# Kernel tuning notes

Hardware: AMD Instinct MI355X
Metric: run time of the kernel (lower is better)

Reference implementation:

```python
import jax, jax.numpy as jnp
import numpy as np
from jax import lax

EMBED_DIM = 384
NUM_GROUPS = 128
GROUP_SIZE = 64
LN_EPS = 1e-5


def setup_inputs() -> dict:
    key = jax.random.key(0)
    k_pts, k1, k2, k3, k4 = jax.random.split(key, 5)
    B, N = 32, 16384
    points = jax.random.normal(k_pts, (B, N, 3), dtype=jnp.float32)
    # local_mlp: Linear(3,128) -> GELU -> Linear(128, embed_dim)
    w1 = jax.random.normal(k1, (3, 128), dtype=jnp.float32) * (1.0 / np.sqrt(3))
    b1 = jax.random.normal(k2, (128,), dtype=jnp.float32) * 0.01
    w2 = jax.random.normal(k3, (128, EMBED_DIM), dtype=jnp.float32) * (1.0 / np.sqrt(128))
    b2 = jax.random.normal(k4, (EMBED_DIM,), dtype=jnp.float32) * 0.01
    ln_scale = jnp.ones((EMBED_DIM,), dtype=jnp.float32)
    ln_bias = jnp.zeros((EMBED_DIM,), dtype=jnp.float32)
    return {"points": points, "w1": w1, "b1": b1, "w2": w2, "b2": b2,
            "ln_scale": ln_scale, "ln_bias": ln_bias}


def _farthest_point_sample(points, num_samples):
    # points: [B, N, 3]. Deterministic start at index 0 (torch uses randint).
    B, N, _ = points.shape

    def step(carry, _):
        distance, farthest = carry  # [B, N], [B]
        centroid = jnp.take_along_axis(points, farthest[:, None, None], axis=1)  # [B,1,3]
        d = jnp.sum((points - centroid) ** 2, axis=-1)  # [B, N]
        distance = jnp.minimum(distance, d)
        nxt = jnp.argmax(distance, axis=-1).astype(jnp.int32)
        return (distance, nxt), farthest

    init = (jnp.full((B, N), jnp.inf, dtype=points.dtype),
            jnp.zeros((B,), dtype=jnp.int32))
    _, idx = lax.scan(step, init, None, length=num_samples)  # [S, B]
    return idx.T  # [B, S]


def reference(points, w1, b1, w2, b2, ln_scale, ln_bias):
    B, N, _ = points.shape
    centroid_idx = _farthest_point_sample(points, NUM_GROUPS)  # [B, G]
    centroids = jnp.take_along_axis(
        points, centroid_idx[:, :, None].astype(jnp.int32), axis=1)  # [B, G, 3]

    # squared distances (same ordering as torch.cdist for topk); matmul form
    # avoids materializing a [B, G, N, 3] diff tensor.
    c2 = jnp.sum(centroids ** 2, axis=-1)  # [B, G]
    p2 = jnp.sum(points ** 2, axis=-1)     # [B, N]
    dist2 = c2[:, :, None] + p2[:, None, :] - 2.0 * jnp.einsum(
        'bgc,bnc->bgn', centroids, points)  # [B, G, N]

    # k smallest -> top_k of negated distances
    _, neighbor_idx = lax.top_k(-dist2, GROUP_SIZE)  # [B, G, K]

    batch_ix = jnp.arange(B)[:, None, None]
    grouped = points[batch_ix, neighbor_idx]  # [B, G, K, 3]
    local_coords = grouped - centroids[:, :, None, :]  # [B, G, K, 3]

    h = jax.nn.gelu(local_coords @ w1 + b1, approximate=False)  # [B,G,K,128]
    feats = h @ w2 + b2  # [B, G, K, D]
    tokens = jnp.mean(feats, axis=2)  # [B, G, D]

    mu = jnp.mean(tokens, axis=-1, keepdims=True)
    var = jnp.mean((tokens - mu) ** 2, axis=-1, keepdims=True)
    tokens_ln = (tokens - mu) * lax.rsqrt(var + LN_EPS) * ln_scale + ln_bias
    return centroids, tokens_ln
```

## Files before the change

kernel.cpp:

```cpp
#include <hip/hip_runtime.h>
#include <math.h>

#define BB 32
#define NN 16384
#define GG 128
#define KK 64
#define HH 128
#define DD 384
#define LN_EPS 1e-5f
#define NBUCK 2048
#define CANDCAP 1024

__device__ __forceinline__ float sq3(float x, float y, float z) {
    return __fadd_rn(__fadd_rn(__fmul_rn(x, x), __fmul_rn(y, y)), __fmul_rn(z, z));
}

__global__ void prep_kernel(const float* __restrict__ w2, float* __restrict__ w2t) {
    int i = blockIdx.x * 256 + threadIdx.x;
    if (i < HH * DD) {
        int f = i >> 7;
        int k = i & 127;
        w2t[i] = w2[k * DD + f];
    }
}

__global__ __launch_bounds__(512) void fps_kernel(const float* __restrict__ pts,
                                                  float* __restrict__ cent_out,
                                                  float4* __restrict__ cent_pad) {
    const int b = blockIdx.x;
    const int tid = threadIdx.x;
    const float* p = pts + (size_t)b * NN * 3;

    float x[32], y[32], z[32], dist[32];
#pragma unroll
    for (int j = 0; j < 32; j++) {
        int n = j * 512 + tid;
        x[j] = p[n * 3 + 0];
        y[j] = p[n * 3 + 1];
        z[j] = p[n * 3 + 2];
        dist[j] = INFINITY;
    }

    __shared__ float cenx, ceny, cenz;
    __shared__ float wv[8];
    __shared__ int wi[8];

    if (tid == 0) { cenx = p[0]; ceny = p[1]; cenz = p[2]; }
    __syncthreads();

    for (int it = 0; it < GG; it++) {
        float cx = cenx, cy = ceny, cz = cenz;
        if (tid == 0) {
            float* co = cent_out + ((size_t)b * GG + it) * 3;
            co[0] = cx; co[1] = cy; co[2] = cz;
            cent_pad[b * GG + it] = make_float4(cx, cy, cz, sq3(cx, cy, cz));
        }
        float bv0 = -INFINITY, bv1 = -INFINITY, bv2 = -INFINITY, bv3 = -INFINITY;
        int bi0 = 0, bi1 = 0, bi2 = 0, bi3 = 0;
#pragma unroll
        for (int j = 0; j < 32; j++) {
            float dx = __fsub_rn(x[j], cx);
            float dy = __fsub_rn(y[j], cy);
            float dz = __fsub_rn(z[j], cz);
            float d = sq3(dx, dy, dz);
            float dj = fminf(dist[j], d);
            dist[j] = dj;
            int n = j * 512 + tid;
            switch (j & 3) {
                case 0: if (dj > bv0) { bv0 = dj; bi0 = n; } break;
                case 1: if (dj > bv1) { bv1 = dj; bi1 = n; } break;
                case 2: if (dj > bv2) { bv2 = dj; bi2 = n; } break;
                case 3: if (dj > bv3) { bv3 = dj; bi3 = n; } break;
            }
        }
        float fv = bv0; int fi = bi0;
        if (bv1 > fv || (bv1 == fv && bi1 < fi)) { fv = bv1; fi = bi1; }
        if (bv2 > fv || (bv2 == fv && bi2 < fi)) { fv = bv2; fi = bi2; }
        if (bv3 > fv || (bv3 == fv && bi3 < fi)) { fv = bv3; fi = bi3; }
#pragma unroll
        for (int off = 32; off >= 1; off >>= 1) {
            float ov = __shfl_down(fv, off);
            int oi = __shfl_down(fi, off);
            if (ov > fv || (ov == fv && oi < fi)) { fv = ov; fi = oi; }
        }
        int lane = tid & 63, wid = tid >> 6;
        if (lane == 0) { wv[wid] = fv; wi[wid] = fi; }
        __syncthreads();
        if (tid == 0) {
            float gv = wv[0]; int gi = wi[0];
            for (int w = 1; w < 8; w++) {
                if (wv[w] > gv || (wv[w] == gv && wi[w] < gi)) { gv = wv[w]; gi = wi[w]; }
            }
            const float* wp = p + (size_t)gi * 3;
            cenx = wp[0]; ceny = wp[1]; cenz = wp[2];
        }
        __syncthreads();
    }
}

__global__ __launch_bounds__(256) void group_kernel(
    const float* __restrict__ pts, const float4* __restrict__ cent_pad,
    const float* __restrict__ w1, const float* __restrict__ b1,
    const float* __restrict__ w2t, const float* __restrict__ b2,
    const float* __restrict__ lns, const float* __restrict__ lnb,
    float* __restrict__ tok_out) {
    __shared__ __align__(16) unsigned hist[NBUCK];
    __shared__ unsigned long long cand[CANDCAP];
    __shared__ int selIdx[KK];
    __shared__ float4 localPt[KK];
    __shared__ float w1s[3 * HH];
    __shared__ float b1s[HH];
    __shared__ __align__(16) float hbar[HH];
    __shared__ float partial[256];
    __shared__ float red2[8];
    __shared__ float toks[DD];
    __shared__ int waveSum[4];
    __shared__ unsigned long long wmin[4];
    __shared__ unsigned TA_S;
    __shared__ int cntS;
    __shared__ unsigned long long lastS;
    __shared__ float muS, rstdS;

    const int tid = threadIdx.x;
    int bid = blockIdx.x;
    int xcd = bid & 7, sub = bid >> 3;
    int b = xcd * 4 + (sub >> 7);
    int g = sub & 127;

    const float* p = pts + (size_t)b * NN * 3;
    float4 c4 = cent_pad[b * GG + g];

    for (int i = tid; i < 3 * HH; i += 256) w1s[i] = w1[i];
    if (tid < HH) b1s[tid] = b1[tid];
    for (int i = tid; i < NBUCK; i += 256) hist[i] = 0;
    if (tid == 0) cntS = 0;
    __syncthreads();

    unsigned key[64];
#pragma unroll
    for (int i = 0; i < 64; i++) {
        int n = i * 256 + tid;
        float px = p[n * 3], py = p[n * 3 + 1], pz = p[n * 3 + 2];
        float p2 = sq3(px, py, pz);
        float dot = __fadd_rn(__fadd_rn(__fmul_rn(c4.x, px), __fmul_rn(c4.y, py)),
                              __fmul_rn(c4.z, pz));
        float d = __fsub_rn(__fadd_rn(c4.w, p2), __fmul_rn(2.0f, dot));
        unsigned u = __float_as_uint(d);
        u ^= (u & 0x80000000u) ? 0xFFFFFFFFu : 0x80000000u;
        key[i] = u;
        atomicAdd(&hist[u >> 21], 1u);
    }
    __syncthreads();

    {
        uint4 h0 = ((const uint4*)hist)[tid * 2];
        uint4 h1 = ((const uint4*)hist)[tid * 2 + 1];
        int loc[8] = {(int)h0.x, (int)h0.y, (int)h0.z, (int)h0.w,
                      (int)h1.x, (int)h1.y, (int)h1.z, (int)h1.w};
        int s = 0;
#pragma unroll
        for (int j = 0; j < 8; j++) s += loc[j];
        int lane = tid & 63, wid = tid >> 6;
        int v = s;
#pragma unroll
        for (int off = 1; off < 64; off <<= 1) {
            int o = __shfl_up(v, off);
            if (lane >= off) v += o;
        }
        if (lane == 63) waveSum[wid] = v;
        __syncthreads();
        int base = 0;
        for (int w = 0; w < wid; w++) base += waveSum[w];
        int c = base + v - s;
#pragma unroll
        for (int j = 0; j < 8; j++) {
            if (c < KK && c + loc[j] >= KK) TA_S = (unsigned)(tid * 8 + j);
            c += loc[j];
        }
        __syncthreads();
    }
    unsigned TA = TA_S;

#pragma unroll
    for (int i = 0; i < 64; i++) {
        unsigned u = key[i];
        if ((u >> 21) <= TA) {
            int pos = atomicAdd(&cntS, 1);
            if (pos < CANDCAP)
                cand[pos] = ((unsigned long long)u << 32) | (unsigned)(i * 256 + tid);
        }
    }
    __syncthreads();
    int cnt = cntS;

    if (cnt <= CANDCAP) {
        for (int c0 = tid; c0 < cnt; c0 += 256) {
            unsigned long long pr = cand[c0];
            int rank = 0;
            for (int j = 0; j < cnt; j++) rank += (cand[j] < pr);
            if (rank < KK) selIdx[rank] = (int)(unsigned)pr;
        }
        __syncthreads();
    } else {
        if (tid == 0) lastS = 0ull;
        __syncthreads();
        for (int r = 0; r < KK; r++) {
            unsigned long long last = lastS;
            unsigned long long best = 0xFFFFFFFFFFFFFFFFull;
#pragma unroll
            for (int i = 0; i < 64; i++) {
                unsigned long long pr =
                    ((unsigned long long)key[i] << 32) | (unsigned)(i * 256 + tid);
                if ((r == 0 || pr > last) && pr < best) best = pr;
            }
            unsigned blo = (unsigned)best, bhi = (unsigned)(best >> 32);
#pragma unroll
            for (int off = 32; off >= 1; off >>= 1) {
                unsigned olo = __shfl_down(blo, off);
                unsigned ohi = __shfl_down(bhi, off);
                unsigned long long ob = ((unsigned long long)ohi << 32) | olo;
                unsigned long long cur = ((unsigned long long)bhi << 32) | blo;
                if (ob < cur) { blo = olo; bhi = ohi; }
            }
            int lane = tid & 63, wid = tid >> 6;
            if (lane == 0) wmin[wid] = ((unsigned long long)bhi << 32) | blo;
            __syncthreads();
            if (tid == 0) {
                unsigned long long m = wmin[0];
                for (int w = 1; w < 4; w++) if (wmin[w] < m) m = wmin[w];
                selIdx[r] = (int)(unsigned)m;
                lastS = m;
            }
            __syncthreads();
        }
    }

    if (tid < KK) {
        int n = selIdx[tid];
        float px = p[n * 3], py = p[n * 3 + 1], pz = p[n * 3 + 2];
        localPt[tid] = make_float4(px - c4.x, py - c4.y, pz - c4.z, 0.f);
    }
    __syncthreads();
    {
        int f = tid & 127, half = tid >> 7;
        float wa = w1s[f], wb = w1s[HH + f], wc = w1s[2 * HH + f], bb = b1s[f];
        float s = 0.f;
        for (int k = half * 32; k < half * 32 + 32; k++) {
            float4 lp = localPt[k];
            float a = lp.x * wa + lp.y * wb + lp.z * wc + bb;
            float hh = 0.5f * a * (1.0f + erff(a * 0.70710678118654752440f));
            s += hh;
        }
        partial[tid] = s;
    }
    __syncthreads();
    if (tid < HH) hbar[tid] = (partial[tid] + partial[tid + HH]) * (1.0f / 64.0f);
    __syncthreads();
    for (int f2 = tid; f2 < DD; f2 += 256) {
        const float4* wrow = (const float4*)(w2t + f2 * HH);
        const float4* hb = (const float4*)hbar;
        float acc = b2[f2];
#pragma unroll 8
        for (int q = 0; q < 32; q++) {
            float4 w4 = wrow[q];
            float4 h4 = hb[q];
            acc += h4.x * w4.x + h4.y * w4.y + h4.z * w4.z + h4.w * w4.w;
        }
        toks[f2] = acc;
    }
    __syncthreads();
    {
        float s1 = 0.f, s2 = 0.f;
        for (int f2 = tid; f2 < DD; f2 += 256) {
            float v = toks[f2];
            s1 += v;
            s2 += v * v;
        }
#pragma unroll
        for (int off = 32; off >= 1; off >>= 1) {
            s1 += __shfl_down(s1, off);
            s2 += __shfl_down(s2, off);
        }
        int lane = tid & 63, wid = tid >> 6;
        if (lane == 0) { partial[wid] = s1; red2[wid] = s2; }
        __syncthreads();
        if (tid == 0) {
            float t1 = partial[0] + partial[1] + partial[2] + partial[3];
            float t2 = red2[0] + red2[1] + red2[2] + red2[3];
            float mu = t1 / (float)DD;
            float var = t2 / (float)DD - mu * mu;
            muS = mu;
            rstdS = rsqrtf(var + LN_EPS);
        }
        __syncthreads();
    }
    float mu = muS, rstd = rstdS;
    float* outp = tok_out + ((size_t)b * GG + g) * DD;
    for (int f2 = tid; f2 < DD; f2 += 256) {
        outp[f2] = (toks[f2] - mu) * rstd * lns[f2] + lnb[f2];
    }
}

extern "C" void kernel_launch(void* const* d_in, const int* in_sizes, int n_in,
                              void* d_out, int out_size, void* d_ws, size_t ws_size,
                              hipStream_t stream) {
    const float* pts = (const float*)d_in[0];
    const float* w1 = (const float*)d_in[1];
    const float* b1 = (const float*)d_in[2];
    const float* w2 = (const float*)d_in[3];
    const float* b2 = (const float*)d_in[4];
    const float* lns = (const float*)d_in[5];
    const float* lnb = (const float*)d_in[6];
    float* out = (float*)d_out;

    float4* cent_pad = (float4*)d_ws;
    float* w2t = (float*)((char*)d_ws + BB * GG * sizeof(float4));

    prep_kernel<<<192, 256, 0, stream>>>(w2, w2t);
    fps_kernel<<<BB, 512, 0, stream>>>(pts, out, cent_pad);
    group_kernel<<<BB * GG, 256, 0, stream>>>(pts, cent_pad, w1, b1, w2t, b2, lns, lnb,
                                              out + BB * GG * 3);
}
```

Measured before the change: 629.9 us.

## Vectorize point loads, single-sync FPS argmax, recompute keys instead of registers

```diff
diff --git a/kernel.cpp b/kernel.cpp
--- a/kernel.cpp
+++ b/kernel.cpp
@@ -15,6 +15,15 @@
     return __fadd_rn(__fadd_rn(__fmul_rn(x, x), __fmul_rn(y, y)), __fmul_rn(z, z));
 }
 
+__device__ __forceinline__ unsigned distkey(float px, float py, float pz, float4 c4) {
+    float p2 = sq3(px, py, pz);
+    float dot = __fadd_rn(__fadd_rn(__fmul_rn(c4.x, px), __fmul_rn(c4.y, py)),
+                          __fmul_rn(c4.z, pz));
+    float d = __fsub_rn(__fadd_rn(c4.w, p2), __fmul_rn(2.0f, dot));
+    unsigned u = __float_as_uint(d);
+    return u ^ ((u & 0x80000000u) ? 0xFFFFFFFFu : 0x80000000u);
+}
+
 __global__ void prep_kernel(const float* __restrict__ w2, float* __restrict__ w2t) {
     int i = blockIdx.x * 256 + threadIdx.x;
     if (i < HH * DD) {
@@ -24,53 +33,62 @@
     }
 }
 
-__global__ __launch_bounds__(512) void fps_kernel(const float* __restrict__ pts,
-                                                  float* __restrict__ cent_out,
-                                                  float4* __restrict__ cent_pad) {
+__global__ __launch_bounds__(512, 2) void fps_kernel(const float* __restrict__ pts,
+                                                     float* __restrict__ cent_out,
+                                                     float4* __restrict__ cent_pad) {
     const int b = blockIdx.x;
     const int tid = threadIdx.x;
     const float* p = pts + (size_t)b * NN * 3;
+    const float4* p4 = (const float4*)p;
 
     float x[32], y[32], z[32], dist[32];
 #pragma unroll
-    for (int j = 0; j < 32; j++) {
-        int n = j * 512 + tid;
-        x[j] = p[n * 3 + 0];
-        y[j] = p[n * 3 + 1];
-        z[j] = p[n * 3 + 2];
-        dist[j] = INFINITY;
-    }
-
-    __shared__ float cenx, ceny, cenz;
-    __shared__ float wv[8];
-    __shared__ int wi[8];
-
-    if (tid == 0) { cenx = p[0]; ceny = p[1]; cenz = p[2]; }
-    __syncthreads();
+    for (int j = 0; j < 8; j++) {
+        int q = j * 512 + tid;
+        float4 A = p4[3 * q], B = p4[3 * q + 1], C = p4[3 * q + 2];
+        x[j * 4 + 0] = A.x; y[j * 4 + 0] = A.y; z[j * 4 + 0] = A.z;
+        x[j * 4 + 1] = A.w; y[j * 4 + 1] = B.x; z[j * 4 + 1] = B.y;
+        x[j * 4 + 2] = B.z; y[j * 4 + 2] = B.w; z[j * 4 + 2] = C.x;
+        x[j * 4 + 3] = C.y; y[j * 4 + 3] = C.z; z[j * 4 + 3] = C.w;
+#pragma unroll
+        for (int t = 0; t < 4; t++) dist[j * 4 + t] = INFINITY;
+    }
+
+    __shared__ unsigned long long slot[GG];
+    for (int i = tid; i < GG; i += 512) slot[i] = 0ull;
+    __syncthreads();
+
+    float cx = p[0], cy = p[1], cz = p[2];
 
     for (int it = 0; it < GG; it++) {
-        float cx = cenx, cy = ceny, cz = cenz;
         if (tid == 0) {
             float* co = cent_out + ((size_t)b * GG + it) * 3;
             co[0] = cx; co[1] = cy; co[2] = cz;
             cent_pad[b * GG + it] = make_float4(cx, cy, cz, sq3(cx, cy, cz));
         }
+        if (it == GG - 1) break;
+
         float bv0 = -INFINITY, bv1 = -INFINITY, bv2 = -INFINITY, bv3 = -INFINITY;
         int bi0 = 0, bi1 = 0, bi2 = 0, bi3 = 0;
 #pragma unroll
-        for (int j = 0; j < 32; j++) {
-            float dx = __fsub_rn(x[j], cx);
-            float dy = __fsub_rn(y[j], cy);
-            float dz = __fsub_rn(z[j], cz);
-            float d = sq3(dx, dy, dz);
-            float dj = fminf(dist[j], d);
-            dist[j] = dj;
-            int n = j * 512 + tid;
-            switch (j & 3) {
-                case 0: if (dj > bv0) { bv0 = dj; bi0 = n; } break;
-                case 1: if (dj > bv1) { bv1 = dj; bi1 = n; } break;
-                case 2: if (dj > bv2) { bv2 = dj; bi2 = n; } break;
-                case 3: if (dj > bv3) { bv3 = dj; bi3 = n; } break;
+        for (int j = 0; j < 8; j++) {
+            int nb = 4 * (j * 512 + tid);
+#pragma unroll
+            for (int t = 0; t < 4; t++) {
+                int r = j * 4 + t;
+                float dx = __fsub_rn(x[r], cx);
+                float dy = __fsub_rn(y[r], cy);
+                float dz = __fsub_rn(z[r], cz);
+                float d = sq3(dx, dy, dz);
+                float dj = fminf(dist[r], d);
+                dist[r] = dj;
+                int n = nb + t;
+                switch (t) {
+                    case 0: if (dj > bv0) { bv0 = dj; bi0 = n; } break;
+                    case 1: if (dj > bv1) { bv1 = dj; bi1 = n; } break;
+                    case 2: if (dj > bv2) { bv2 = dj; bi2 = n; } break;
+                    case 3: if (dj > bv3) { bv3 = dj; bi3 = n; } break;
+                }
             }
         }
         float fv = bv0; int fi = bi0;
@@ -83,29 +101,30 @@
             int oi = __shfl_down(fi, off);
             if (ov > fv || (ov == fv && oi < fi)) { fv = ov; fi = oi; }
         }
-        int lane = tid & 63, wid = tid >> 6;
-        if (lane == 0) { wv[wid] = fv; wi[wid] = fi; }
-        __syncthreads();
-        if (tid == 0) {
-            float gv = wv[0]; int gi = wi[0];
-            for (int w = 1; w < 8; w++) {
-                if (wv[w] > gv || (wv[w] == gv && wi[w] < gi)) { gv = wv[w]; gi = wi[w]; }
-            }
-            const float* wp = p + (size_t)gi * 3;
-            cenx = wp[0]; ceny = wp[1]; cenz = wp[2];
-        }
-        __syncthreads();
-    }
-}
-
-__global__ __launch_bounds__(256) void group_kernel(
+        if ((tid & 63) == 0) {
+            unsigned long long packed =
+                ((unsigned long long)__float_as_uint(fv) << 32) |
+                (unsigned)(0xFFFFFFFFu - (unsigned)fi);
+            atomicMax(&slot[it], packed);
+        }
+        __syncthreads();
+        unsigned long long w = slot[it];
+        int idx = (int)(0xFFFFFFFFu - (unsigned)w);
+        const float* wp = p + (size_t)idx * 3;
+        cx = wp[0]; cy = wp[1]; cz = wp[2];
+    }
+}
+
+__global__ __launch_bounds__(256, 6) void group_kernel(
     const float* __restrict__ pts, const float4* __restrict__ cent_pad,
     const float* __restrict__ w1, const float* __restrict__ b1,
     const float* __restrict__ w2t, const float* __restrict__ b2,
     const float* __restrict__ lns, const float* __restrict__ lnb,
     float* __restrict__ tok_out) {
-    __shared__ __align__(16) unsigned hist[NBUCK];
-    __shared__ unsigned long long cand[CANDCAP];
+    __shared__ __align__(16) union {
+        unsigned hist[NBUCK];
+        unsigned long long cand[CANDCAP];
+    } sh;
     __shared__ int selIdx[KK];
     __shared__ float4 localPt[KK];
     __shared__ float w1s[3 * HH];
@@ -128,33 +147,32 @@
     int g = sub & 127;
 
     const float* p = pts + (size_t)b * NN * 3;
+    const float4* p4 = (const float4*)p;
     float4 c4 = cent_pad[b * GG + g];
 
     for (int i = tid; i < 3 * HH; i += 256) w1s[i] = w1[i];
     if (tid < HH) b1s[tid] = b1[tid];
-    for (int i = tid; i < NBUCK; i += 256) hist[i] = 0;
+    for (int i = tid; i < NBUCK; i += 256) sh.hist[i] = 0;
     if (tid == 0) cntS = 0;
     __syncthreads();
 
-    unsigned key[64];
-#pragma unroll
-    for (int i = 0; i < 64; i++) {
-        int n = i * 256 + tid;
-        float px = p[n * 3], py = p[n * 3 + 1], pz = p[n * 3 + 2];
-        float p2 = sq3(px, py, pz);
-        float dot = __fadd_rn(__fadd_rn(__fmul_rn(c4.x, px), __fmul_rn(c4.y, py)),
-                              __fmul_rn(c4.z, pz));
-        float d = __fsub_rn(__fadd_rn(c4.w, p2), __fmul_rn(2.0f, dot));
-        unsigned u = __float_as_uint(d);
-        u ^= (u & 0x80000000u) ? 0xFFFFFFFFu : 0x80000000u;
-        key[i] = u;
-        atomicAdd(&hist[u >> 21], 1u);
+    for (int i = 0; i < 16; i++) {
+        int t4 = i * 256 + tid;
+        float4 A = p4[3 * t4], B = p4[3 * t4 + 1], C = p4[3 * t4 + 2];
+        unsigned k0 = distkey(A.x, A.y, A.z, c4);
+        unsigned k1 = distkey(A.w, B.x, B.y, c4);
+        unsigned k2 = distkey(B.z, B.w, C.x, c4);
+        unsigned k3 = distkey(C.y, C.z, C.w, c4);
+        atomicAdd(&sh.hist[k0 >> 21], 1u);
+        atomicAdd(&sh.hist[k1 >> 21], 1u);
+        atomicAdd(&sh.hist[k2 >> 21], 1u);
+        atomicAdd(&sh.hist[k3 >> 21], 1u);
     }
     __syncthreads();
 
     {
-        uint4 h0 = ((const uint4*)hist)[tid * 2];
-        uint4 h1 = ((const uint4*)hist)[tid * 2 + 1];
+        uint4 h0 = ((const uint4*)sh.hist)[tid * 2];
+        uint4 h1 = ((const uint4*)sh.hist)[tid * 2 + 1];
         int loc[8] = {(int)h0.x, (int)h0.y, (int)h0.z, (int)h0.w,
                       (int)h1.x, (int)h1.y, (int)h1.z, (int)h1.w};
         int s = 0;
@@ -181,13 +199,22 @@
     }
     unsigned TA = TA_S;
 
-#pragma unroll
-    for (int i = 0; i < 64; i++) {
-        unsigned u = key[i];
-        if ((u >> 21) <= TA) {
-            int pos = atomicAdd(&cntS, 1);
-            if (pos < CANDCAP)
-                cand[pos] = ((unsigned long long)u << 32) | (unsigned)(i * 256 + tid);
+    for (int i = 0; i < 16; i++) {
+        int t4 = i * 256 + tid;
+        float4 A = p4[3 * t4], B = p4[3 * t4 + 1], C = p4[3 * t4 + 2];
+        unsigned k[4];
+        k[0] = distkey(A.x, A.y, A.z, c4);
+        k[1] = distkey(A.w, B.x, B.y, c4);
+        k[2] = distkey(B.z, B.w, C.x, c4);
+        k[3] = distkey(C.y, C.z, C.w, c4);
+#pragma unroll
+        for (int q = 0; q < 4; q++) {
+            if ((k[q] >> 21) <= TA) {
+                int pos = atomicAdd(&cntS, 1);
+                if (pos < CANDCAP)
+                    sh.cand[pos] =
+                        ((unsigned long long)k[q] << 32) | (unsigned)(4 * t4 + q);
+            }
         }
     }
     __syncthreads();
@@ -195,9 +222,9 @@
 
     if (cnt <= CANDCAP) {
         for (int c0 = tid; c0 < cnt; c0 += 256) {
-            unsigned long long pr = cand[c0];
+            unsigned long long pr = sh.cand[c0];
             int rank = 0;
-            for (int j = 0; j < cnt; j++) rank += (cand[j] < pr);
+            for (int j = 0; j < cnt; j++) rank += (sh.cand[j] < pr);
             if (rank < KK) selIdx[rank] = (int)(unsigned)pr;
         }
         __syncthreads();
@@ -207,11 +234,20 @@
         for (int r = 0; r < KK; r++) {
             unsigned long long last = lastS;
             unsigned long long best = 0xFFFFFFFFFFFFFFFFull;
-#pragma unroll
-            for (int i = 0; i < 64; i++) {
-                unsigned long long pr =
-                    ((unsigned long long)key[i] << 32) | (unsigned)(i * 256 + tid);
-                if ((r == 0 || pr > last) && pr < best) best = pr;
+            for (int i = 0; i < 16; i++) {
+                int t4 = i * 256 + tid;
+                float4 A = p4[3 * t4], B = p4[3 * t4 + 1], C = p4[3 * t4 + 2];
+                unsigned k[4];
+                k[0] = distkey(A.x, A.y, A.z, c4);
+                k[1] = distkey(A.w, B.x, B.y, c4);
+                k[2] = distkey(B.z, B.w, C.x, c4);
+                k[3] = distkey(C.y, C.z, C.w, c4);
+#pragma unroll
+                for (int q = 0; q < 4; q++) {
+                    unsigned long long pr =
+                        ((unsigned long long)k[q] << 32) | (unsigned)(4 * t4 + q);
+                    if ((r == 0 || pr > last) && pr < best) best = pr;
+                }
             }
             unsigned blo = (unsigned)best, bhi = (unsigned)(best >> 32);
 #pragma unroll
```

New measurement: 533.6 us. 1.18x faster.
